# Kernel tuning notes

Measured on AMD Instinct MI355X. Metric: run time of the kernel, lower is better.

## Reference

```python
import jax, jax.numpy as jnp
import numpy as np

B, T, N, A, D, S, E, H = 32, 64, 16, 20, 128, 32, 64, 256  # batch, time, n_agents, n_actions, state_dim, sample_size, embed_dim, hypernet_embed


def _lin(k, fi, fo):
    return jax.random.normal(k, (fi, fo), jnp.float32) / np.sqrt(fi)


def setup_inputs() -> dict:
    key = jax.random.key(0)
    ks = jax.random.split(key, 16)
    batch = B * T
    states = jax.random.normal(ks[0], (B, T, D), jnp.float32)
    a_idx = jax.random.randint(ks[1], (B, T, N), 0, A)
    actions = jax.nn.one_hot(a_idx, A, dtype=jnp.float32)
    agent_qs = jax.random.normal(ks[2], (B, T, N), jnp.float32)
    max_filter = jnp.zeros((B, T, N), jnp.float32)
    # random agent permutations (torch.multinomial without replacement)
    grand_coalitions = jnp.argsort(jax.random.uniform(ks[3], (batch * S, N)), axis=1).astype(jnp.int32)
    return {
        "states": states, "actions": actions, "agent_qs": agent_qs,
        "max_filter": max_filter, "grand_coalitions": grand_coalitions,
        # hyper_w_1: Linear(D,H) -> ReLU -> Linear(H, E*2A)
        "W1a": _lin(ks[4], D, H), "b1a": jnp.zeros((H,), jnp.float32),
        "W1b": _lin(ks[5], H, E * 2 * A), "b1b": jnp.zeros((E * 2 * A,), jnp.float32),
        # hyper_b_1: Linear(D,E)
        "Wb": _lin(ks[6], D, E), "bb": jnp.zeros((E,), jnp.float32),
        # hyper_w_final: Linear(D,H) -> ReLU -> Linear(H,E)
        "Wfa": _lin(ks[7], D, H), "bfa": jnp.zeros((H,), jnp.float32),
        "Wfb": _lin(ks[8], H, E), "bfb": jnp.zeros((E,), jnp.float32),
        # V: Linear(D,E) -> ReLU -> Linear(E,1)
        "Wv1": _lin(ks[9], D, E), "bv1": jnp.zeros((E,), jnp.float32),
        "Wv2": _lin(ks[10], E, 1), "bv2": jnp.zeros((1,), jnp.float32),
    }


def reference(states, actions, agent_qs, max_filter, grand_coalitions,
              W1a, b1a, W1b, b1b, Wb, bb, Wfa, bfa, Wfb, bfb, Wv1, bv1, Wv2, bv2):
    b, t = states.shape[0], states.shape[1]
    batch = b * t
    n, a = actions.shape[2], actions.shape[3]
    s = grand_coalitions.shape[0] // batch
    e = Wb.shape[1]

    st = states.reshape(batch, -1)                      # [batch, D]
    act = actions.reshape(batch, n, a)                  # [batch, N, A]
    gc = grand_coalitions.reshape(batch, s, n)          # [batch, S, N]

    # individual_map one-hot + tril matmul => subcoalition; mask = sub - ind = (j < gc)
    j = jnp.arange(n)
    sub = (j[None, None, None, :] <= gc[..., None]).astype(st.dtype)   # [batch,S,N,N]
    ind = (j[None, None, None, :] == gc[..., None]).astype(st.dtype)
    mask = sub - ind                                                    # [batch,S,i,j]

    # gathered (permuted) actions: perm_act[b,s,j,:] = act[b, gc[b,s,j], :]
    perm_act = act[jnp.arange(batch)[:, None, None], gc]                # [batch,S,N,A]

    # mean over coalition axis j of masked actions, times coalition size, mean over samples
    numer = jnp.einsum('bsij,bsja->bsia', mask, perm_act)               # sum_j masked actions
    cnt = mask.sum(-1)                                                  # [batch,S,N]
    coal = ((numer / n) * cnt[..., None]).mean(axis=1)                  # [batch,N,A]

    # per (batch, agent) hypernetwork mixing
    inputs = jnp.concatenate([coal, act], axis=-1).reshape(batch * n, 2 * a)  # [bn, 2A]
    st_rep = jnp.broadcast_to(st[:, None, :], (batch, n, st.shape[-1])).reshape(batch * n, -1)

    def mlp2(x, Wa_, ba_, Wb_, bb_):
        return jax.nn.relu(x @ Wa_ + ba_) @ Wb_ + bb_

    w1 = jnp.abs(mlp2(st_rep, W1a, b1a, W1b, b1b)).reshape(-1, 2 * a, e)      # [bn,2A,E]
    b1 = (st_rep @ Wb + bb)                                                   # [bn,E]
    hidden = jax.nn.elu(jnp.einsum('bk,bke->be', inputs, w1) + b1)            # [bn,E]
    w_final = jnp.abs(mlp2(st_rep, Wfa, bfa, Wfb, bfb))                       # [bn,E]
    v = jax.nn.relu(st_rep @ Wv1 + bv1) @ Wv2 + bv2                           # [bn,1]
    y = jnp.sum(hidden * w_final, axis=-1, keepdims=True) + v                 # [bn,1]
    w_est = jnp.abs(y).reshape(b, t, n)

    q_tot = jnp.sum(w_est * agent_qs, axis=2, keepdims=True)                  # [B,T,1]
    return q_tot, w_est
```

## Files before the change

### kernel.cpp

```cpp
#include <hip/hip_runtime.h>
#include <math.h>


#define BATCH 2048

typedef __attribute__((ext_vector_type(8))) short bf16x8;
typedef __attribute__((ext_vector_type(4))) float f32x4;

__device__ inline unsigned short f2bf(float f) {
    unsigned int u = __float_as_uint(f);
    unsigned int r = (u + 0x7FFFu + ((u >> 16) & 1u)) >> 16;
    return (unsigned short)r;
}
__device__ inline float bf2f(unsigned short s) {
    return __uint_as_float(((unsigned int)s) << 16);
}

__global__ __launch_bounds__(256) void k1(
    const float* __restrict__ X,
    const float* __restrict__ W1a, const float* __restrict__ b1a,
    const float* __restrict__ Wfa, const float* __restrict__ bfa,
    const float* __restrict__ Wb,  const float* __restrict__ bb,
    const float* __restrict__ Wv1, const float* __restrict__ bv1,
    const float* __restrict__ W1b,
    const float* __restrict__ actions, const int* __restrict__ gc,
    unsigned short* __restrict__ h1_bf, float* __restrict__ hf,
    float* __restrict__ b1buf, float* __restrict__ vrelu,
    unsigned short* __restrict__ Bp,
    float* __restrict__ coal, int* __restrict__ arowbuf)
{
    __shared__ __align__(16) char smem[8192];
    const int t = threadIdx.x, bid = blockIdx.x;

    if (bid >= 640) {
        int b = bid - 640;
        int* q            = (int*)smem;
        unsigned int* msk = (unsigned int*)(smem + 2048);
        int* aidx         = (int*)(smem + 2048 + 2560);

        if (t < 128) ((uint4*)q)[t] = ((const uint4*)(gc + b * 512))[t];
        if (t < 160) ((uint4*)msk)[t] = make_uint4(0u, 0u, 0u, 0u);
        {
            float av = actions[b * 320 + t];
            if (av > 0.5f) aidx[t / 20] = t % 20;
        }
        if (t < 64) {
            float av = actions[b * 320 + 256 + t];
            if (av > 0.5f) aidx[(256 + t) / 20] = (256 + t) % 20;
        }
        __syncthreads();
        if (t < 16) arowbuf[b * 16 + t] = 20 + aidx[t];
        {
            int s = t >> 4, j = t & 15;
            atomicOr(&msk[s * 20 + aidx[q[s * 16 + j]]], 1u << j);
            s += 16;
            atomicOr(&msk[s * 20 + aidx[q[s * 16 + j]]], 1u << j);
        }
        __syncthreads();
        for (int u = t; u < 320; u += 256) {
            int i = u / 20, a = u % 20;
            float acc = 0.f;
            #pragma unroll 8
            for (int s = 0; s < 32; ++s) {
                int g = q[s * 16 + i];
                acc += (float)(g * __popc(msk[s * 20 + a] & ((1u << g) - 1u)));
            }
            coal[(b * 16 + i) * 20 + a] = acc * (1.0f / 512.0f);
        }
        return;
    }

    if (bid >= 320) {
        int idx = (bid - 320) * 256 + t;
        int n_local = idx & 127;
        int g = idx >> 7;
        int kg = g & 3, kcn = g >> 2;
        int kc = kcn & 7, nb = kcn >> 3;
        int kbase = kc * 32 + kg * 8;
        int col = nb * 128 + n_local;
        unsigned short o[8];
        #pragma unroll
        for (int j = 0; j < 8; ++j)
            o[j] = f2bf(W1b[(kbase + j) * 2560 + col]);
        *(uint4*)&Bp[idx * 8] = *(uint4*)o;
        return;
    }

    float (*As)[64] = (float(*)[64])smem;
    float (*Bs)[64] = (float(*)[64])(smem + 4096);

    const int nb = bid % 10, mb = bid / 10;
    const int m0 = mb * 64, n0 = nb * 64;
    const int tx = t & 15, ty = t >> 4;
    const int lm = t >> 2, lk = (t & 3) << 2;
    const int lkk = t >> 4, lnb = (t & 15) << 2;

    const float* Wsrc; const float* bsrc; int ldb, c0;
    if (nb < 4)       { Wsrc = W1a; bsrc = b1a; ldb = 256; c0 = n0; }
    else if (nb < 8)  { Wsrc = Wfa; bsrc = bfa; ldb = 256; c0 = n0 - 256; }
    else if (nb == 8) { Wsrc = Wb;  bsrc = bb;  ldb = 64;  c0 = 0; }
    else              { Wsrc = Wv1; bsrc = bv1; ldb = 64;  c0 = 0; }

    float c[4][4] = {{0}};
    for (int k0 = 0; k0 < 128; k0 += 16) {
        float4 av = *(const float4*)&X[(m0 + lm) * 128 + k0 + lk];
        As[lk][lm] = av.x; As[lk+1][lm] = av.y; As[lk+2][lm] = av.z; As[lk+3][lm] = av.w;
        *(float4*)&Bs[lkk][lnb] = *(const float4*)&Wsrc[(k0 + lkk) * ldb + c0 + lnb];
        __syncthreads();
        #pragma unroll
        for (int kk = 0; kk < 16; ++kk) {
            float4 a4 = *(const float4*)&As[kk][ty * 4];
            float4 b4 = *(const float4*)&Bs[kk][tx * 4];
            float aa[4] = {a4.x, a4.y, a4.z, a4.w};
            float bb4[4] = {b4.x, b4.y, b4.z, b4.w};
            #pragma unroll
            for (int i = 0; i < 4; ++i)
                #pragma unroll
                for (int j = 0; j < 4; ++j)
                    c[i][j] = fmaf(aa[i], bb4[j], c[i][j]);
        }
        __syncthreads();
    }
    const int ncol = c0 + tx * 4;
    float4 bias = *(const float4*)&bsrc[ncol];
    #pragma unroll
    for (int i = 0; i < 4; ++i) {
        int m = m0 + ty * 4 + i;
        float v0 = c[i][0] + bias.x, v1 = c[i][1] + bias.y;
        float v2 = c[i][2] + bias.z, v3 = c[i][3] + bias.w;
        if (nb < 4) {
            ushort4 o;
            o.x = f2bf(fmaxf(v0, 0.f)); o.y = f2bf(fmaxf(v1, 0.f));
            o.z = f2bf(fmaxf(v2, 0.f)); o.w = f2bf(fmaxf(v3, 0.f));
            *(ushort4*)&h1_bf[m * 256 + ncol] = o;
        } else if (nb < 8) {
            float4 o = { fmaxf(v0,0.f), fmaxf(v1,0.f), fmaxf(v2,0.f), fmaxf(v3,0.f) };
            *(float4*)&hf[m * 256 + ncol] = o;
        } else if (nb == 8) {
            float4 o = { v0, v1, v2, v3 };
            *(float4*)&b1buf[m * 64 + ncol] = o;
        } else {
            float4 o = { fmaxf(v0,0.f), fmaxf(v1,0.f), fmaxf(v2,0.f), fmaxf(v3,0.f) };
            *(float4*)&vrelu[m * 64 + ncol] = o;
        }
    }
}

#define AS_STRIDE 40
__global__ __launch_bounds__(256) void k2(
    const unsigned short* __restrict__ A, const unsigned short* __restrict__ Bp,
    const float* __restrict__ bias, unsigned short* __restrict__ C,
    const float* __restrict__ hf, const float* __restrict__ Wfb,
    const float* __restrict__ bfb, float* __restrict__ wf)
{
    __shared__ __align__(16) char smem[18432];
    const int t = threadIdx.x, bid = blockIdx.x;

    if (bid < 320) {
        unsigned short* As = (unsigned short*)smem;
        unsigned short* Bs = (unsigned short*)(smem + 10240);
        const int lane = t & 63, wave = t >> 6;
        const int ln15 = lane & 15, q4 = lane >> 4;
        const int nb = bid % 20, m0 = (bid / 20) * 128, n0 = nb * 128;
        const int wm = (wave & 1) * 64, wn = (wave >> 1) * 64;

        f32x4 acc[4][4];
        #pragma unroll
        for (int i = 0; i < 4; ++i)
            #pragma unroll
            for (int j = 0; j < 4; ++j)
                acc[i][j] = (f32x4){0.f, 0.f, 0.f, 0.f};

        for (int kc = 0; kc < 8; ++kc) {
            #pragma unroll
            for (int c = 0; c < 2; ++c) {
                int ch = t + c * 256;
                int row = ch >> 2, part = ch & 3;
                *(uint4*)&As[row * AS_STRIDE + part * 8] =
                    *(const uint4*)&A[(m0 + row) * 256 + kc * 32 + part * 8];
            }
            {
                const uint4* src = (const uint4*)&Bp[(nb * 8 + kc) * 4096];
                ((uint4*)Bs)[t] = src[t];
                ((uint4*)Bs)[t + 256] = src[t + 256];
            }
            __syncthreads();
            bf16x8 af[4], bfr[4];
            #pragma unroll
            for (int mi = 0; mi < 4; ++mi)
                af[mi] = *(const bf16x8*)&As[(wm + mi * 16 + ln15) * AS_STRIDE + q4 * 8];
            #pragma unroll
            for (int ni = 0; ni < 4; ++ni)
                bfr[ni] = *(const bf16x8*)&Bs[(q4 * 128 + wn + ni * 16 + ln15) * 8];
            #pragma unroll
            for (int mi = 0; mi < 4; ++mi)
                #pragma unroll
                for (int ni = 0; ni < 4; ++ni)
                    acc[mi][ni] = __builtin_amdgcn_mfma_f32_16x16x32_bf16(af[mi], bfr[ni], acc[mi][ni], 0, 0, 0);
            __syncthreads();
        }
        #pragma unroll
        for (int ni = 0; ni < 4; ++ni) {
            int col = n0 + wn + ni * 16 + ln15;
            float bv = bias[col];
            #pragma unroll
            for (int mi = 0; mi < 4; ++mi) {
                #pragma unroll
                for (int j = 0; j < 4; ++j) {
                    int row = m0 + wm + mi * 16 + q4 * 4 + j;
                    C[row * 2560 + col] = f2bf(fabsf(acc[mi][ni][j] + bv));
                }
            }
        }
    } else {
        float* hfs  = (float*)smem;
        float* wfbs = (float*)(smem + 2048);
        const int e = t & 63, mg = t >> 6;
        const int b0 = (bid - 320) * 8;
        float acc0 = 0.f, acc1 = 0.f;

        for (int kc = 0; kc < 4; ++kc) {
            for (int i = t; i < 1024; i += 256)
                ((float4*)wfbs)[i] = ((const float4*)(Wfb + kc * 64 * 64))[i];
            if (t < 128) {
                int r = t >> 4, p = t & 15;
                ((float4*)hfs)[t] = *(const float4*)&hf[(b0 + r) * 256 + kc * 64 + p * 4];
            }
            __syncthreads();
            #pragma unroll 8
            for (int k = 0; k < 64; ++k) {
                float wv = wfbs[k * 64 + e];
                acc0 = fmaf(hfs[mg * 64 + k], wv, acc0);
                acc1 = fmaf(hfs[(mg + 4) * 64 + k], wv, acc1);
            }
            __syncthreads();
        }
        float bf = bfb[e];
        wf[(b0 + mg) * 64 + e]     = fabsf(acc0 + bf);
        wf[(b0 + mg + 4) * 64 + e] = fabsf(acc1 + bf);
    }
}

__global__ __launch_bounds__(512) void k3(
    const float* __restrict__ coal, const int* __restrict__ arowbuf,
    const unsigned short* __restrict__ w1, const float* __restrict__ b1buf,
    const float* __restrict__ wf, const float* __restrict__ vrelu,
    const float* __restrict__ Wv2, const float* __restrict__ bv2,
    const float* __restrict__ agent_qs, float* __restrict__ out)
{
    __shared__ unsigned short w1s[1280];
    __shared__ float ins[16][20];
    __shared__ int arow[16];
    __shared__ float wq[16];
    const int t = threadIdx.x, b = blockIdx.x;

    if (t < 160) {
        ((uint4*)w1s)[t] = ((const uint4*)(w1 + b * 2560))[t];
    } else if (t < 480) {
        ((float*)ins)[t - 160] = coal[b * 320 + (t - 160)];
    } else if (t < 496) {
        arow[t - 480] = arowbuf[b * 16 + (t - 480)];
    }
    __syncthreads();

    const int e = t & 63, wv = t >> 6;
    const float b1v = b1buf[b * 64 + e];
    const float wfv = wf[b * 64 + e];
    const float vv  = vrelu[b * 64 + e] * Wv2[e];
    const float b2  = bv2[0];

    #pragma unroll
    for (int pass = 0; pass < 2; ++pass) {
        const int i = wv + pass * 8;
        float acc = b1v;
        #pragma unroll
        for (int k = 0; k < 20; ++k)
            acc = fmaf(ins[i][k], bf2f(w1s[k * 64 + e]), acc);
        acc += bf2f(w1[b * 2560 + arow[i] * 64 + e]);
        float hidden = acc > 0.f ? acc : expm1f(acc);
        float p = hidden * wfv + vv;
        #pragma unroll
        for (int off = 32; off > 0; off >>= 1)
            p += __shfl_down(p, off, 64);
        if (e == 0) {
            float west = fabsf(p + b2);
            out[2048 + b * 16 + i] = west;
            wq[i] = west * agent_qs[b * 16 + i];
        }
    }
    __syncthreads();
    if (t < 16) {
        float v = wq[t];
        v += __shfl_down(v, 8, 64);
        v += __shfl_down(v, 4, 64);
        v += __shfl_down(v, 2, 64);
        v += __shfl_down(v, 1, 64);
        if (t == 0) out[b] = v;
    }
}

extern "C" void kernel_launch(void* const* d_in, const int* in_sizes, int n_in,
                              void* d_out, int out_size, void* d_ws, size_t ws_size,
                              hipStream_t stream) {
    const float* states   = (const float*)d_in[0];
    const float* actions  = (const float*)d_in[1];
    const float* agent_qs = (const float*)d_in[2];
    const int*   gc       = (const int*)d_in[4];
    const float* W1a = (const float*)d_in[5];
    const float* b1a = (const float*)d_in[6];
    const float* W1b = (const float*)d_in[7];
    const float* b1b = (const float*)d_in[8];
    const float* Wb  = (const float*)d_in[9];
    const float* bb  = (const float*)d_in[10];
    const float* Wfa = (const float*)d_in[11];
    const float* bfa = (const float*)d_in[12];
    const float* Wfb = (const float*)d_in[13];
    const float* bfb = (const float*)d_in[14];
    const float* Wv1 = (const float*)d_in[15];
    const float* bv1 = (const float*)d_in[16];
    const float* Wv2 = (const float*)d_in[17];
    const float* bv2 = (const float*)d_in[18];

    float* ws     = (float*)d_ws;
    float* hf     = ws;
    float* b1buf  = hf + 524288;
    float* vrelu  = b1buf + 131072;
    float* wfbuf  = vrelu + 131072;
    unsigned short* h1_bf = (unsigned short*)(wfbuf + 131072);
    unsigned short* Bp    = h1_bf + 524288;
    unsigned short* w1    = Bp + 655360;
    float* coal   = (float*)(w1 + 5242880);
    int*   arowbuf = (int*)(coal + 655360);
    float* out = (float*)d_out;

    k1<<<2688, 256, 0, stream>>>(states, W1a, b1a, Wfa, bfa, Wb, bb, Wv1, bv1,
                                 W1b, actions, gc, h1_bf, hf, b1buf, vrelu, Bp,
                                 coal, arowbuf);
    k2<<<576, 256, 0, stream>>>(h1_bf, Bp, b1b, w1, hf, Wfb, bfb, wfbuf);
    k3<<<BATCH, 512, 0, stream>>>(coal, arowbuf, w1, b1buf, wfbuf, vrelu,
                                  Wv2, bv2, agent_qs, out);
}
```

Baseline: 132.3 us.

## Double-buffer GEMM tiles with register prefetch and stage bf16 output through LDS

In k1, the next k-slice of X and the weights is loaded into registers before the FMA loop runs, so global latency overlaps compute. In the bf16 MFMA GEMM of k2, A/B tiles are double-buffered in LDS, with the next chunk loaded into registers during the MFMAs and written afterwards, which removes one barrier per iteration. The k2 epilogue now writes results to an LDS tile and then stores 16-byte coalesced rows, instead of scattered 2-byte global stores. LDS use in k2 doubles to 36 KB, which may reduce occupancy, and register pressure rises.

```diff
diff --git a/kernel.cpp b/kernel.cpp
--- a/kernel.cpp
+++ b/kernel.cpp
@@ -102,11 +102,16 @@
     else              { Wsrc = Wv1; bsrc = bv1; ldb = 64;  c0 = 0; }
 
     float c[4][4] = {{0}};
+    float4 av = *(const float4*)&X[(m0 + lm) * 128 + lk];
+    float4 bv = *(const float4*)&Wsrc[lkk * ldb + c0 + lnb];
     for (int k0 = 0; k0 < 128; k0 += 16) {
-        float4 av = *(const float4*)&X[(m0 + lm) * 128 + k0 + lk];
         As[lk][lm] = av.x; As[lk+1][lm] = av.y; As[lk+2][lm] = av.z; As[lk+3][lm] = av.w;
-        *(float4*)&Bs[lkk][lnb] = *(const float4*)&Wsrc[(k0 + lkk) * ldb + c0 + lnb];
-        __syncthreads();
+        *(float4*)&Bs[lkk][lnb] = bv;
+        __syncthreads();
+        if (k0 < 112) {
+            av = *(const float4*)&X[(m0 + lm) * 128 + k0 + 16 + lk];
+            bv = *(const float4*)&Wsrc[(k0 + 16 + lkk) * ldb + c0 + lnb];
+        }
         #pragma unroll
         for (int kk = 0; kk < 16; ++kk) {
             float4 a4 = *(const float4*)&As[kk][ty * 4];
@@ -147,22 +152,26 @@
 }
 
 #define AS_STRIDE 40
+#define CS_STRIDE 136
 __global__ __launch_bounds__(256) void k2(
     const unsigned short* __restrict__ A, const unsigned short* __restrict__ Bp,
     const float* __restrict__ bias, unsigned short* __restrict__ C,
     const float* __restrict__ hf, const float* __restrict__ Wfb,
     const float* __restrict__ bfb, float* __restrict__ wf)
 {
-    __shared__ __align__(16) char smem[18432];
+    __shared__ __align__(16) char smem[36864];
     const int t = threadIdx.x, bid = blockIdx.x;
 
     if (bid < 320) {
-        unsigned short* As = (unsigned short*)smem;
-        unsigned short* Bs = (unsigned short*)(smem + 10240);
+        unsigned short* AsB[2] = { (unsigned short*)smem,
+                                   (unsigned short*)(smem + 10240) };
+        unsigned short* BsB[2] = { (unsigned short*)(smem + 20480),
+                                   (unsigned short*)(smem + 28672) };
         const int lane = t & 63, wave = t >> 6;
         const int ln15 = lane & 15, q4 = lane >> 4;
         const int nb = bid % 20, m0 = (bid / 20) * 128, n0 = nb * 128;
         const int wm = (wave & 1) * 64, wn = (wave >> 1) * 64;
+        const int row0 = t >> 2, part0 = t & 3;
 
         f32x4 acc[4][4];
         #pragma unroll
@@ -171,46 +180,74 @@
             for (int j = 0; j < 4; ++j)
                 acc[i][j] = (f32x4){0.f, 0.f, 0.f, 0.f};
 
+        *(uint4*)&AsB[0][row0 * AS_STRIDE + part0 * 8] =
+            *(const uint4*)&A[(m0 + row0) * 256 + part0 * 8];
+        *(uint4*)&AsB[0][(row0 + 64) * AS_STRIDE + part0 * 8] =
+            *(const uint4*)&A[(m0 + row0 + 64) * 256 + part0 * 8];
+        {
+            const uint4* src = (const uint4*)&Bp[(nb * 8) * 4096];
+            ((uint4*)BsB[0])[t] = src[t];
+            ((uint4*)BsB[0])[t + 256] = src[t + 256];
+        }
+        __syncthreads();
+
         for (int kc = 0; kc < 8; ++kc) {
-            #pragma unroll
-            for (int c = 0; c < 2; ++c) {
-                int ch = t + c * 256;
-                int row = ch >> 2, part = ch & 3;
-                *(uint4*)&As[row * AS_STRIDE + part * 8] =
-                    *(const uint4*)&A[(m0 + row) * 256 + kc * 32 + part * 8];
-            }
-            {
-                const uint4* src = (const uint4*)&Bp[(nb * 8 + kc) * 4096];
-                ((uint4*)Bs)[t] = src[t];
-                ((uint4*)Bs)[t + 256] = src[t + 256];
-            }
-            __syncthreads();
+            unsigned short* Ac = AsB[kc & 1];
+            unsigned short* Bc = BsB[kc & 1];
+            unsigned short* An = AsB[(kc & 1) ^ 1];
+            unsigned short* Bn = BsB[(kc & 1) ^ 1];
+
+            uint4 ra0, ra1, rb0, rb1;
+            if (kc < 7) {
+                ra0 = *(const uint4*)&A[(m0 + row0) * 256 + (kc + 1) * 32 + part0 * 8];
+                ra1 = *(const uint4*)&A[(m0 + row0 + 64) * 256 + (kc + 1) * 32 + part0 * 8];
+                const uint4* src = (const uint4*)&Bp[(nb * 8 + kc + 1) * 4096];
+                rb0 = src[t];
+                rb1 = src[t + 256];
+            }
+
             bf16x8 af[4], bfr[4];
             #pragma unroll
             for (int mi = 0; mi < 4; ++mi)
-                af[mi] = *(const bf16x8*)&As[(wm + mi * 16 + ln15) * AS_STRIDE + q4 * 8];
+                af[mi] = *(const bf16x8*)&Ac[(wm + mi * 16 + ln15) * AS_STRIDE + q4 * 8];
             #pragma unroll
             for (int ni = 0; ni < 4; ++ni)
-                bfr[ni] = *(const bf16x8*)&Bs[(q4 * 128 + wn + ni * 16 + ln15) * 8];
+                bfr[ni] = *(const bf16x8*)&Bc[(q4 * 128 + wn + ni * 16 + ln15) * 8];
             #pragma unroll
             for (int mi = 0; mi < 4; ++mi)
                 #pragma unroll
                 for (int ni = 0; ni < 4; ++ni)
                     acc[mi][ni] = __builtin_amdgcn_mfma_f32_16x16x32_bf16(af[mi], bfr[ni], acc[mi][ni], 0, 0, 0);
+
+            if (kc < 7) {
+                *(uint4*)&An[row0 * AS_STRIDE + part0 * 8] = ra0;
+                *(uint4*)&An[(row0 + 64) * AS_STRIDE + part0 * 8] = ra1;
+                ((uint4*)Bn)[t] = rb0;
+                ((uint4*)Bn)[t + 256] = rb1;
+            }
             __syncthreads();
         }
+
+        unsigned short* Cs = (unsigned short*)smem;
         #pragma unroll
         for (int ni = 0; ni < 4; ++ni) {
-            int col = n0 + wn + ni * 16 + ln15;
-            float bv = bias[col];
+            int coll = wn + ni * 16 + ln15;
+            float bv = bias[n0 + coll];
             #pragma unroll
             for (int mi = 0; mi < 4; ++mi) {
                 #pragma unroll
                 for (int j = 0; j < 4; ++j) {
-                    int row = m0 + wm + mi * 16 + q4 * 4 + j;
-                    C[row * 2560 + col] = f2bf(fabsf(acc[mi][ni][j] + bv));
+                    int rowl = wm + mi * 16 + q4 * 4 + j;
+                    Cs[rowl * CS_STRIDE + coll] = f2bf(fabsf(acc[mi][ni][j] + bv));
                 }
             }
+        }
+        __syncthreads();
+        #pragma unroll
+        for (int u = t; u < 2048; u += 256) {
+            int row = u >> 4, c8 = (u & 15) << 3;
+            *(uint4*)&C[(m0 + row) * 2560 + n0 + c8] =
+                *(const uint4*)&Cs[row * CS_STRIDE + c8];
         }
     } else {
         float* hfs  = (float*)smem;
```

Result: no change. 130.0 us (median of 2 runs) (-1.8%).
